# Performance work log

Measured on AMD Instinct MI355X. Metric: run time of the kernel, lower is better.

The kernel has to match this reference:

```python
import jax, jax.numpy as jnp
import numpy as np

B, N, M = 4, 8192, 8192


def setup_inputs() -> dict:
    key = jax.random.key(0)
    k1, k2 = jax.random.split(key)
    xyz1 = jax.random.normal(k1, (B, N, 3), dtype=jnp.float32)
    xyz2 = jax.random.normal(k2, (B, M, 3), dtype=jnp.float32)
    return {"xyz1": xyz1, "xyz2": xyz2}


def _chamfer(xyz1, xyz2):
    # Squared Euclidean pairwise distances via the expansion
    # ||a-b||^2 = ||a||^2 + ||b||^2 - 2 a.b  (avoids a [B,N,M,3] diff tensor).
    sq1 = jnp.sum(xyz1 * xyz1, axis=-1)              # [B,N]
    sq2 = jnp.sum(xyz2 * xyz2, axis=-1)              # [B,M]
    inner = jnp.einsum('bnd,bmd->bnm', xyz1, xyz2)   # [B,N,M]
    d = sq1[:, :, None] + sq2[:, None, :] - 2.0 * inner
    d = jnp.maximum(d, 0.0)
    dist1 = jnp.min(d, axis=2)  # [B,N] nearest xyz2 point for each xyz1 point
    dist2 = jnp.min(d, axis=1)  # [B,M] nearest xyz1 point for each xyz2 point
    return dist1, dist2


def reference(xyz1, xyz2):
    return _chamfer(xyz1, xyz2)
```

## Files before the change

kernel.cpp:

```cpp
#include <hip/hip_runtime.h>


typedef __bf16 bf16_t;
typedef __bf16 bf16x8 __attribute__((ext_vector_type(8)));
typedef float  f32x16 __attribute__((ext_vector_type(16)));

#define NPTS    8192
#define NB      4
#define NSETPTS (NB * NPTS)
#define TPB     256
#define WAVES   4
#define QC      (WAVES * 32)
#define QPANELS (NPTS / QC)
#define SEGR    16
#define RC      (NPTS / SEGR)
#define RT      (RC / 32)
#define NSLOT   (RC * 2)

__global__ void chamfer_init_out(unsigned int* __restrict__ out, int n) {
    int i = blockIdx.x * blockDim.x + threadIdx.x;
    if (i < n) out[i] = 0x7F800000u;
}

__device__ __forceinline__ void gload16(const bf16_t* g, bf16_t* l) {
    __builtin_amdgcn_global_load_lds(
        (const __attribute__((address_space(1))) void*)g,
        (__attribute__((address_space(3))) void*)l, 16, 0, 0);
}

__device__ __forceinline__ void split2(float v, bf16_t& h, bf16_t& l) {
    h = (bf16_t)v;
    l = (bf16_t)(v - (float)h);
}

__device__ __forceinline__ float tree16(const f32x16& x) {
    float a = fminf(fminf(x[0],  x[1]),  x[2]);
    float b = fminf(fminf(x[3],  x[4]),  x[5]);
    float c = fminf(fminf(x[6],  x[7]),  x[8]);
    float d = fminf(fminf(x[9],  x[10]), x[11]);
    float e = fminf(fminf(x[12], x[13]), x[14]);
    a = fminf(fminf(a, b), x[15]);
    c = fminf(fminf(c, d), e);
    return fminf(a, c);
}

__global__ void chamfer_prep(const float* __restrict__ xyz1,
                             const float* __restrict__ xyz2,
                             bf16_t* __restrict__ a16,
                             bf16_t* __restrict__ b16) {
    int i = blockIdx.x * blockDim.x + threadIdx.x;
    const int perm[16] = {0,1,2,3, 8,9,10,11, 4,5,6,7, 12,13,14,15};

    {
        float x = xyz1[3 * i], y = xyz1[3 * i + 1], z = xyz1[3 * i + 2];
        float sq = x * x + y * y + z * z;
        bf16_t m2xh, m2xl, m2yh, m2yl, m2zh, m2zl, sqh, sql;
        split2(-2.f * x, m2xh, m2xl);
        split2(-2.f * y, m2yh, m2yl);
        split2(-2.f * z, m2zh, m2zl);
        split2(sq, sqh, sql);
        bf16_t one = (bf16_t)1.0f, zero = (bf16_t)0.0f;
        bf16_t A[16] = { m2xh, m2yh, m2zh,  m2xl, m2yl, m2zl,
                         m2xh, m2yh, m2zh,  sqh, sql, one, one, zero, zero, zero };
        bf16_t* ao = a16 + (size_t)i * 16;
#pragma unroll
        for (int j = 0; j < 16; ++j) ao[j] = A[perm[j]];
    }

    {
        float x = xyz2[3 * i], y = xyz2[3 * i + 1], z = xyz2[3 * i + 2];
        float sq = x * x + y * y + z * z;
        bf16_t xh, xl, yh, yl, zh, zl, sqh, sql;
        split2(x, xh, xl);
        split2(y, yh, yl);
        split2(z, zh, zl);
        split2(sq, sqh, sql);
        bf16_t one = (bf16_t)1.0f, zero = (bf16_t)0.0f;
        bf16_t Bv[16] = { xh, yh, zh,  xh, yh, zh,  xl, yl, zl,
                          one, one, sqh, sql, zero, zero, zero };
        int p = i & 31;
        size_t tb = (size_t)(i & ~31) * 16;
        int s0 = (2 * p)     ^ (p & 7);
        int s1 = (2 * p + 1) ^ (p & 7);
        bf16_t* bo0 = b16 + tb + (size_t)s0 * 8;
        bf16_t* bo1 = b16 + tb + (size_t)s1 * 8;
#pragma unroll
        for (int j = 0; j < 8; ++j) bo0[j] = Bv[perm[j]];
#pragma unroll
        for (int j = 0; j < 8; ++j) bo1[j] = Bv[perm[j + 8]];
    }
}

__global__ __launch_bounds__(TPB) void chamfer_main(
    const bf16_t* __restrict__ a16,
    const bf16_t* __restrict__ b16,
    unsigned int* __restrict__ out)
{
    __shared__ __align__(16) unsigned char smem[WAVES * 32 * 33 * 4];
    __shared__ unsigned int colmin[RC];
    bf16_t* sbuf = (bf16_t*)smem;
    float (*red)[32][33] = (float (*)[32][33])smem;

    int bid = blockIdx.x;
    int s   = bid & (SEGR - 1);    bid >>= 4;
    int qp  = bid & (QPANELS - 1); bid >>= 6;
    int b   = bid;

    int wave = threadIdx.x >> 6;
    int lane = threadIdx.x & 63;
    int col  = lane & 31;
    int h    = lane >> 5;

    const bf16_t* ap = a16 + (size_t)b * NPTS * 16;
    const bf16_t* gB = b16 + (size_t)(b * NPTS + s * RC) * 16;

#pragma unroll
    for (int c = 0; c < 4; ++c) {
        int slot = c * 256 + threadIdx.x;
        gload16(gB + (size_t)slot * 8, sbuf + (size_t)slot * 8);
    }

#pragma unroll
    for (int k = 0; k < RC / TPB; ++k)
        colmin[k * TPB + threadIdx.x] = 0x7F800000u;

    int qbase = qp * QC + wave * 32;
    bf16x8 af = *((const bf16x8*)(ap + (size_t)(qbase + col) * 16) + h);

    f32x16 rm, zacc;
#pragma unroll
    for (int g = 0; g < 16; ++g) { rm[g] = INFINITY; zacc[g] = 0.f; }

    __syncthreads();

    int swz = ((2 * col + h) ^ (col & 7)) * 8;
    const bf16_t* sl = sbuf + swz;

#pragma unroll 1
    for (int t = 0; t < RT; t += 2) {
        bf16x8 c0 = *(const bf16x8*)(sl + (size_t)(t + 0) * 512);
        bf16x8 c1 = *(const bf16x8*)(sl + (size_t)(t + 1) * 512);

        f32x16 x0 = __builtin_amdgcn_mfma_f32_32x32x16_bf16(af, c0, zacc, 0, 0, 0);
        f32x16 x1 = __builtin_amdgcn_mfma_f32_32x32x16_bf16(af, c1, zacc, 0, 0, 0);

#pragma unroll
        for (int g = 0; g < 16; ++g) rm[g] = fminf(fminf(x0[g], x1[g]), rm[g]);

        float s0 = tree16(x0);
        float s1 = tree16(x1);
        float m0 = fminf(s0, __shfl_xor(s0, 32));
        float m1 = fminf(s1, __shfl_xor(s1, 32));
        m0 = fmaxf(m0, 0.f);
        m1 = fmaxf(m1, 0.f);
        if (h == 0) {
            atomicMin(&colmin[t * 32 + col],       __float_as_uint(m0));
            atomicMin(&colmin[(t + 1) * 32 + col], __float_as_uint(m1));
        }
    }

    __syncthreads();

    {
        int out2base = NSETPTS + b * NPTS + s * RC;
#pragma unroll
        for (int k = 0; k < RC / TPB; ++k) {
            int j = k * TPB + threadIdx.x;
            atomicMin(&out[out2base + j], colmin[j]);
        }
    }

#pragma unroll
    for (int g = 0; g < 16; ++g) {
        int row = (g & 3) + 8 * (g >> 2) + 4 * h;
        red[wave][row][col] = rm[g];
    }
    __syncthreads();

    if (threadIdx.x < QC) {
        int w = threadIdx.x >> 5, r = threadIdx.x & 31;
        const float* rp = &red[w][r][0];
        float v0 = rp[0], v1 = rp[1], v2 = rp[2], v3 = rp[3];
#pragma unroll
        for (int cc = 4; cc < 32; cc += 4) {
            v0 = fminf(v0, rp[cc + 0]);
            v1 = fminf(v1, rp[cc + 1]);
            v2 = fminf(v2, rp[cc + 2]);
            v3 = fminf(v3, rp[cc + 3]);
        }
        float v = fmaxf(fminf(fminf(v0, v1), fminf(v2, v3)), 0.f);
        atomicMin(&out[b * NPTS + qp * QC + threadIdx.x], __float_as_uint(v));
    }
}

extern "C" void kernel_launch(void* const* d_in, const int* in_sizes, int n_in,
                              void* d_out, int out_size, void* d_ws, size_t ws_size,
                              hipStream_t stream) {
    const float* xyz1 = (const float*)d_in[0];
    const float* xyz2 = (const float*)d_in[1];
    unsigned int* out = (unsigned int*)d_out;

    bf16_t* a16 = (bf16_t*)d_ws;
    bf16_t* b16 = a16 + (size_t)NSETPTS * 16;

    hipLaunchKernelGGL(chamfer_init_out,
                       dim3((out_size + TPB - 1) / TPB), dim3(TPB), 0, stream,
                       out, out_size);

    hipLaunchKernelGGL(chamfer_prep,
                       dim3(NSETPTS / TPB), dim3(TPB), 0, stream,
                       xyz1, xyz2, a16, b16);

    hipLaunchKernelGGL(chamfer_main,
                       dim3(NB * QPANELS * SEGR), dim3(TPB), 0, stream,
                       a16, b16, out);
}
```

Baseline: 79.44 us.

## Replace global atomicMin with per-block partial writes and a separate reduce kernel

Each main-kernel block now stores its row and column partial minima to workspace instead of issuing global atomicMin to the output. A new reduce kernel then takes the min over the 16 segments for dist1 and over the 64 query panels for dist2. This also removes the init kernel. It is meant to remove contention and latency from global atomics, at the cost of extra workspace traffic (about 8 MB written and read for dist2) and one extra launch.

Result: slower. 83.02 us (+4.5%).

```diff
diff --git a/kernel.cpp b/kernel.cpp
--- a/kernel.cpp
+++ b/kernel.cpp
@@ -16,11 +16,6 @@
 #define RC      (NPTS / SEGR)
 #define RT      (RC / 32)
 #define NSLOT   (RC * 2)
-
-__global__ void chamfer_init_out(unsigned int* __restrict__ out, int n) {
-    int i = blockIdx.x * blockDim.x + threadIdx.x;
-    if (i < n) out[i] = 0x7F800000u;
-}
 
 __device__ __forceinline__ void gload16(const bf16_t* g, bf16_t* l) {
     __builtin_amdgcn_global_load_lds(
@@ -94,7 +89,8 @@
 __global__ __launch_bounds__(TPB) void chamfer_main(
     const bf16_t* __restrict__ a16,
     const bf16_t* __restrict__ b16,
-    unsigned int* __restrict__ out)
+    unsigned int* __restrict__ wsd1,
+    unsigned int* __restrict__ wsd2)
 {
     __shared__ __align__(16) unsigned char smem[WAVES * 32 * 33 * 4];
     __shared__ unsigned int colmin[RC];
@@ -162,11 +158,11 @@
     __syncthreads();
 
     {
-        int out2base = NSETPTS + b * NPTS + s * RC;
+        unsigned int* d2 = wsd2 + ((size_t)(b * SEGR + s) * QPANELS + qp) * RC;
 #pragma unroll
         for (int k = 0; k < RC / TPB; ++k) {
             int j = k * TPB + threadIdx.x;
-            atomicMin(&out[out2base + j], colmin[j]);
+            d2[j] = colmin[j];
         }
     }
 
@@ -189,7 +185,32 @@
             v3 = fminf(v3, rp[cc + 3]);
         }
         float v = fmaxf(fminf(fminf(v0, v1), fminf(v2, v3)), 0.f);
-        atomicMin(&out[b * NPTS + qp * QC + threadIdx.x], __float_as_uint(v));
+        wsd1[((size_t)(b * QPANELS + qp) * SEGR + s) * QC + threadIdx.x] =
+            __float_as_uint(v);
+    }
+}
+
+__global__ void chamfer_reduce(const unsigned int* __restrict__ wsd1,
+                               const unsigned int* __restrict__ wsd2,
+                               unsigned int* __restrict__ out) {
+    int i = blockIdx.x * blockDim.x + threadIdx.x;
+    if (i < NSETPTS) {
+        int b = i >> 13, q = i & (NPTS - 1);
+        int qp = q >> 7, qi = q & (QC - 1);
+        const unsigned int* p = wsd1 + ((size_t)(b * QPANELS + qp) * SEGR) * QC + qi;
+        unsigned int m = 0x7F800000u;
+#pragma unroll
+        for (int s = 0; s < SEGR; ++s) m = min(m, p[(size_t)s * QC]);
+        out[i] = m;
+    } else {
+        int i2 = i - NSETPTS;
+        int b = i2 >> 13, r = i2 & (NPTS - 1);
+        int s = r >> 9, rj = r & (RC - 1);
+        const unsigned int* p = wsd2 + ((size_t)(b * SEGR + s) * QPANELS) * RC + rj;
+        unsigned int m = 0x7F800000u;
+#pragma unroll
+        for (int qp = 0; qp < QPANELS; ++qp) m = min(m, p[(size_t)qp * RC]);
+        out[NSETPTS + i2] = m;
     }
 }
 
@@ -200,12 +221,11 @@
     const float* xyz2 = (const float*)d_in[1];
     unsigned int* out = (unsigned int*)d_out;
 
-    bf16_t* a16 = (bf16_t*)d_ws;
-    bf16_t* b16 = a16 + (size_t)NSETPTS * 16;
-
-    hipLaunchKernelGGL(chamfer_init_out,
-                       dim3((out_size + TPB - 1) / TPB), dim3(TPB), 0, stream,
-                       out, out_size);
+    unsigned char* ws = (unsigned char*)d_ws;
+    bf16_t* a16        = (bf16_t*)(ws);
+    bf16_t* b16        = (bf16_t*)(ws + (1u << 20));
+    unsigned int* wsd1 = (unsigned int*)(ws + (2u << 20));
+    unsigned int* wsd2 = (unsigned int*)(ws + (4u << 20));
 
     hipLaunchKernelGGL(chamfer_prep,
                        dim3(NSETPTS / TPB), dim3(TPB), 0, stream,
@@ -213,5 +233,9 @@
 
     hipLaunchKernelGGL(chamfer_main,
                        dim3(NB * QPANELS * SEGR), dim3(TPB), 0, stream,
-                       a16, b16, out);
-}
+                       a16, b16, wsd1, wsd2);
+
+    hipLaunchKernelGGL(chamfer_reduce,
+                       dim3(2 * NSETPTS / TPB), dim3(TPB), 0, stream,
+                       wsd1, wsd2, out);
+}
```
